# Performance work log

Measured on AMD Instinct MI355X. Metric: run time of the kernel, lower is better.

Reference implementation:

```python
import jax, jax.numpy as jnp
import numpy as np

EMB = 512
HEAD = 64
B, S = 4, 4096


def setup_inputs() -> dict:
    key = jax.random.key(0)
    kq, kk, kv, kwq, kwk, kwv = jax.random.split(key, 6)
    q = jax.random.normal(kq, (B, S, EMB), dtype=jnp.float32)
    k = jax.random.normal(kk, (B, S, EMB), dtype=jnp.float32)
    v = jax.random.normal(kv, (B, S, EMB), dtype=jnp.float32)
    # nn.Linear weights: [out_features, in_features], no bias
    sc = 1.0 / np.sqrt(EMB)
    Wq = jax.random.uniform(kwq, (HEAD, EMB), jnp.float32, -sc, sc)
    Wk = jax.random.uniform(kwk, (HEAD, EMB), jnp.float32, -sc, sc)
    Wv = jax.random.uniform(kwv, (HEAD, EMB), jnp.float32, -sc, sc)
    return {"q": q, "k": k, "v": v, "Wq": Wq, "Wk": Wk, "Wv": Wv}


def reference(q, k, v, Wq, Wk, Wv):
    scale = 1.0 / np.sqrt(HEAD).astype(np.float32)
    Q = jnp.einsum('bse,he->bsh', q, Wq)  # [B,S,HEAD]
    K = jnp.einsum('bse,he->bsh', k, Wk)
    V = jnp.einsum('bse,he->bsh', v, Wv)
    scores = jnp.einsum('bqh,bkh->bqk', Q, K) * scale  # [B,S,S]
    attn = jax.nn.softmax(scores, axis=-1)
    # dropout p=0.0 -> identity
    out = jnp.einsum('bqk,bkh->bqh', attn, V)  # [B,S,HEAD]
    return out
```

## Files before the change

kernel.cpp:

```cpp
#include <hip/hip_runtime.h>
#include <hip/hip_bf16.h>

#define EMB    512
#define HEAD   64
#define SEQ    4096
#define NB     4
#define NSPLIT 8
#define LDX    72

#define SL2E   0.18033688011112042f

typedef __bf16 bf16x8 __attribute__((ext_vector_type(8)));
typedef float  f32x4  __attribute__((ext_vector_type(4)));

__device__ inline ushort4 cvt4(float4 v) {
    __hip_bfloat16 a = __float2bfloat16(v.x), b = __float2bfloat16(v.y);
    __hip_bfloat16 c = __float2bfloat16(v.z), d = __float2bfloat16(v.w);
    ushort4 r;
    r.x = *(unsigned short*)&a; r.y = *(unsigned short*)&b;
    r.z = *(unsigned short*)&c; r.w = *(unsigned short*)&d;
    return r;
}

__global__ __launch_bounds__(256) void cvtw_kernel(
    const float* __restrict__ Wq, const float* __restrict__ Wk,
    const float* __restrict__ Wv, __hip_bfloat16* __restrict__ Wc)
{
    int idx   = blockIdx.x * 256 + threadIdx.x;
    int which = idx >> 13;
    int off   = (idx & 8191) * 4;
    const float* src = (which == 0) ? Wq : (which == 1) ? Wk : Wv;
    float s = (which == 0) ? SL2E : 1.0f;
    float4 v = *(const float4*)(src + off);
    v.x *= s; v.y *= s; v.z *= s; v.w *= s;
    *(ushort4*)(Wc + which * 64 * EMB + off) = cvt4(v);
}

__global__ __launch_bounds__(256, 3) void proj_kernel(
    const float* __restrict__ q, const float* __restrict__ k, const float* __restrict__ v,
    const __hip_bfloat16* __restrict__ Wc,
    __hip_bfloat16* __restrict__ Qo, __hip_bfloat16* __restrict__ Ko,
    __hip_bfloat16* __restrict__ Vto)
{
    __shared__ __hip_bfloat16 Xs[64][LDX];

    const int which = blockIdx.y;
    const float* __restrict__ x = (which == 0) ? q : (which == 1) ? k : v;
    const __hip_bfloat16* __restrict__ W = Wc + which * 64 * EMB;

    const int tid  = threadIdx.x;
    const int wave = tid >> 6, lane = tid & 63;
    const int l16  = lane & 15, quad = lane >> 4;
    const int r0   = blockIdx.x * 64;
    const float* __restrict__ xb = x + (size_t)r0 * EMB;

    const int sr = tid >> 4;
    const int sc = (tid & 15) << 2;

    const f32x4 z = {0.f, 0.f, 0.f, 0.f};
    f32x4 acc[4] = {z, z, z, z};

    float4 xr[4];
    bf16x8 wf[8];

#define LOADX(dst, e0)                                                        \
    _Pragma("unroll")                                                         \
    for (int it = 0; it < 4; ++it)                                            \
        dst[it] = *(const float4*)(xb + (size_t)(it * 16 + sr) * EMB + (e0) + sc);

#define LOADW(dst, e0)                                                        \
    _Pragma("unroll")                                                         \
    for (int st = 0; st < 2; ++st)                                            \
        _Pragma("unroll")                                                     \
        for (int t = 0; t < 4; ++t)                                           \
            dst[st * 4 + t] = *(const bf16x8*)(W + (size_t)(t * 16 + l16) * EMB \
                                               + (e0) + st * 32 + quad * 8);

    LOADX(xr, 0);
    LOADW(wf, 0);

    #pragma unroll
    for (int c = 0; c < 8; ++c) {
        const int e0 = c * 64;
        if (c) __syncthreads();
        #pragma unroll
        for (int it = 0; it < 4; ++it)
            *(ushort4*)&Xs[it * 16 + sr][sc] = cvt4(xr[it]);
        __syncthreads();

        bf16x8 a0 = *(const bf16x8*)&Xs[wave * 16 + l16][quad * 8];
        bf16x8 a1 = *(const bf16x8*)&Xs[wave * 16 + l16][32 + quad * 8];

        float4 xr2[4];
        bf16x8 wf2[8];
        if (c < 7) { LOADX(xr2, e0 + 64); LOADW(wf2, e0 + 64); }

        #pragma unroll
        for (int t = 0; t < 4; ++t)
            acc[t] = __builtin_amdgcn_mfma_f32_16x16x32_bf16(a0, wf[t], acc[t], 0, 0, 0);
        #pragma unroll
        for (int t = 0; t < 4; ++t)
            acc[t] = __builtin_amdgcn_mfma_f32_16x16x32_bf16(a1, wf[4 + t], acc[t], 0, 0, 0);

        if (c < 7) {
            #pragma unroll
            for (int it = 0; it < 4; ++it) xr[it] = xr2[it];
            #pragma unroll
            for (int j = 0; j < 8; ++j) wf[j] = wf2[j];
        }
    }
#undef LOADX
#undef LOADW

    #pragma unroll
    for (int t = 0; t < 4; ++t) {
        #pragma unroll
        for (int r = 0; r < 4; ++r) {
            int row = r0 + wave * 16 + quad * 4 + r;
            int h   = t * 16 + l16;
            __hip_bfloat16 val = __float2bfloat16(acc[t][r]);
            if (which == 0) {
                Qo[(size_t)row * HEAD + h] = val;
            } else if (which == 1) {
                Ko[(size_t)row * HEAD + h] = val;
            } else {
                int b = row >> 12, s = row & (SEQ - 1);
                Vto[((size_t)b * HEAD + h) * SEQ + s] = val;
            }
        }
    }
}

__global__ __launch_bounds__(256) void attn_kernel(
    const __hip_bfloat16* __restrict__ Qb, const __hip_bfloat16* __restrict__ Kb,
    const __hip_bfloat16* __restrict__ Vt, float* __restrict__ Op,
    float* __restrict__ lp)
{
    __shared__ __hip_bfloat16 QPs[64][LDX];
    __shared__ __hip_bfloat16 Ks[64][LDX];
    __shared__ __hip_bfloat16 Vs[64][LDX];

    const int tid  = threadIdx.x;
    const int wave = tid >> 6, lane = tid & 63;
    const int l16  = lane & 15, quad = lane >> 4;
    const int b    = blockIdx.y;
    const int q0   = blockIdx.x * 64;
    const int split = blockIdx.z;
    const int j0base = split * (SEQ / NSPLIT);

    for (int i = tid; i < 512; i += 256) {
        int r = i >> 3, c8 = (i & 7) * 8;
        *(uint4*)&QPs[r][c8] =
            *(const uint4*)(Qb + ((size_t)b * SEQ + q0 + r) * HEAD + c8);
    }
    __syncthreads();

    bf16x8 qf0 = *(const bf16x8*)&QPs[wave * 16 + l16][quad * 8];
    bf16x8 qf1 = *(const bf16x8*)&QPs[wave * 16 + l16][32 + quad * 8];

    const f32x4 z = {0.f, 0.f, 0.f, 0.f};
    f32x4 oacc[4] = {z, z, z, z};
    float l_r[4] = {0.f, 0.f, 0.f, 0.f};

    for (int jt = 0; jt < SEQ / NSPLIT; jt += 64) {
        const int j0 = j0base + jt;
        __syncthreads();
        for (int i = tid; i < 512; i += 256) {
            int r = i >> 3, c8 = (i & 7) * 8;
            *(uint4*)&Ks[r][c8] =
                *(const uint4*)(Kb + ((size_t)b * SEQ + j0 + r) * HEAD + c8);
            *(uint4*)&Vs[r][c8] =
                *(const uint4*)(Vt + ((size_t)b * HEAD + r) * SEQ + j0 + c8);
        }
        __syncthreads();

        f32x4 sacc[4] = {z, z, z, z};
        #pragma unroll
        for (int st = 0; st < 2; ++st) {
            bf16x8 a = (st == 0) ? qf0 : qf1;
            #pragma unroll
            for (int t = 0; t < 4; ++t) {
                bf16x8 bK = *(const bf16x8*)&Ks[t * 16 + l16][st * 32 + quad * 8];
                sacc[t] = __builtin_amdgcn_mfma_f32_16x16x32_bf16(a, bK, sacc[t], 0, 0, 0);
            }
        }

        #pragma unroll
        for (int r = 0; r < 4; ++r) {
            float ls = 0.f;
            #pragma unroll
            for (int t = 0; t < 4; ++t) {
                float p = __builtin_amdgcn_exp2f(sacc[t][r]);
                ls += p;
                QPs[wave * 16 + quad * 4 + r][t * 16 + l16] = __float2bfloat16(p);
            }
            l_r[r] += ls;
        }

        #pragma unroll
        for (int st = 0; st < 2; ++st) {
            bf16x8 pf = *(const bf16x8*)&QPs[wave * 16 + l16][st * 32 + quad * 8];
            #pragma unroll
            for (int t = 0; t < 4; ++t) {
                bf16x8 vf = *(const bf16x8*)&Vs[t * 16 + l16][st * 32 + quad * 8];
                oacc[t] = __builtin_amdgcn_mfma_f32_16x16x32_bf16(pf, vf, oacc[t], 0, 0, 0);
            }
        }
    }

    #pragma unroll
    for (int r = 0; r < 4; ++r) {
        float s = l_r[r];
        #pragma unroll
        for (int off = 1; off < 16; off <<= 1) s += __shfl_xor(s, off);
        l_r[r] = s;
    }
    const size_t pb = (size_t)(split * NB + b) * SEQ;
    if (l16 == 0) {
        #pragma unroll
        for (int r = 0; r < 4; ++r)
            lp[pb + q0 + wave * 16 + quad * 4 + r] = l_r[r];
    }
    #pragma unroll
    for (int t = 0; t < 4; ++t)
        #pragma unroll
        for (int r = 0; r < 4; ++r)
            Op[(pb + q0 + wave * 16 + quad * 4 + r) * HEAD + t * 16 + l16] = oacc[t][r];
}

__global__ __launch_bounds__(256) void merge_kernel(
    const float* __restrict__ Op, const float* __restrict__ lp,
    float* __restrict__ out)
{
    int idx = blockIdx.x * 256 + threadIdx.x;
    int bq  = idx >> 4;
    int c4  = (idx & 15) * 4;
    float4 acc = {0.f, 0.f, 0.f, 0.f};
    float  l   = 0.f;
    #pragma unroll
    for (int s = 0; s < NSPLIT; ++s) {
        float4 o = *(const float4*)(Op + ((size_t)s * NB * SEQ + bq) * HEAD + c4);
        acc.x += o.x; acc.y += o.y; acc.z += o.z; acc.w += o.w;
        l += lp[(size_t)s * NB * SEQ + bq];
    }
    float inv = 1.f / l;
    float4 r = {acc.x * inv, acc.y * inv, acc.z * inv, acc.w * inv};
    *(float4*)(out + (size_t)bq * HEAD + c4) = r;
}

extern "C" void kernel_launch(void* const* d_in, const int* in_sizes, int n_in,
                              void* d_out, int out_size, void* d_ws, size_t ws_size,
                              hipStream_t stream) {
    const float* q  = (const float*)d_in[0];
    const float* k  = (const float*)d_in[1];
    const float* v  = (const float*)d_in[2];
    const float* Wq = (const float*)d_in[3];
    const float* Wk = (const float*)d_in[4];
    const float* Wv = (const float*)d_in[5];
    float* out = (float*)d_out;

    __hip_bfloat16* Qb = (__hip_bfloat16*)d_ws;
    __hip_bfloat16* Kb = Qb + (size_t)NB * SEQ * HEAD;
    __hip_bfloat16* Vt = Kb + (size_t)NB * SEQ * HEAD;
    __hip_bfloat16* Wc = Vt + (size_t)NB * SEQ * HEAD;
    float* Op = (float*)(Wc + 3 * 64 * EMB);
    float* lp = Op + (size_t)NSPLIT * NB * SEQ * HEAD;

    cvtw_kernel<<<96, 256, 0, stream>>>(Wq, Wk, Wv, Wc);

    dim3 pgrid(NB * SEQ / 64, 3);
    proj_kernel<<<pgrid, dim3(256), 0, stream>>>(q, k, v, Wc, Qb, Kb, Vt);

    dim3 agrid(SEQ / 64, NB, NSPLIT);
    attn_kernel<<<agrid, dim3(256), 0, stream>>>(Qb, Kb, Vt, Op, lp);

    merge_kernel<<<(NB * SEQ * 16) / 256, dim3(256), 0, stream>>>(Op, lp, out);
}
```

Measured before the change: 184.2 us.

## Load K/V fragments directly from global memory and compute row sums via MFMA

Drops the shared-memory staging of Q, K and V tiles and the two block-wide barriers per iteration; each wave now reads its MFMA operand fragments straight from global memory, relying on caches for reuse across the four waves. Row sums of P are now produced by an extra MFMA against a ones vector, taking the same bf16-rounded P as the PV product, instead of fp32 adds plus shuffle reductions. This removes barrier and LDS traffic but replaces coalesced tile loads with strided 16-byte per-lane global loads that each wave repeats, raising L1/L2 pressure and exposing load latency without explicit prefetch.

```diff
diff --git a/kernel.cpp b/kernel.cpp
--- a/kernel.cpp
+++ b/kernel.cpp
@@ -136,43 +136,33 @@
     const __hip_bfloat16* __restrict__ Vt, float* __restrict__ Op,
     float* __restrict__ lp)
 {
-    __shared__ __hip_bfloat16 QPs[64][LDX];
-    __shared__ __hip_bfloat16 Ks[64][LDX];
-    __shared__ __hip_bfloat16 Vs[64][LDX];
+    __shared__ __hip_bfloat16 Ps[64][LDX];
 
     const int tid  = threadIdx.x;
     const int wave = tid >> 6, lane = tid & 63;
     const int l16  = lane & 15, quad = lane >> 4;
     const int b    = blockIdx.y;
     const int q0   = blockIdx.x * 64;
-    const int split = blockIdx.z;
-    const int j0base = split * (SEQ / NSPLIT);
-
-    for (int i = tid; i < 512; i += 256) {
-        int r = i >> 3, c8 = (i & 7) * 8;
-        *(uint4*)&QPs[r][c8] =
-            *(const uint4*)(Qb + ((size_t)b * SEQ + q0 + r) * HEAD + c8);
-    }
-    __syncthreads();
-
-    bf16x8 qf0 = *(const bf16x8*)&QPs[wave * 16 + l16][quad * 8];
-    bf16x8 qf1 = *(const bf16x8*)&QPs[wave * 16 + l16][32 + quad * 8];
+    const int j0b  = blockIdx.z * (SEQ / NSPLIT);
+
+    const __hip_bfloat16* qrow = Qb + ((size_t)b * SEQ + q0 + wave * 16 + l16) * HEAD + quad * 8;
+    bf16x8 qf0 = *(const bf16x8*)(qrow);
+    bf16x8 qf1 = *(const bf16x8*)(qrow + 32);
+
+    const __hip_bfloat16* kbase = Kb + (size_t)b * SEQ * HEAD + quad * 8;
+    const __hip_bfloat16* vbase = Vt + ((size_t)b * HEAD + l16) * SEQ + quad * 8;
 
     const f32x4 z = {0.f, 0.f, 0.f, 0.f};
     f32x4 oacc[4] = {z, z, z, z};
-    float l_r[4] = {0.f, 0.f, 0.f, 0.f};
+    f32x4 lacc = z;
+
+    const __hip_bfloat16 one_bf = __float2bfloat16(1.0f);
+    bf16x8 ones;
+    #pragma unroll
+    for (int j = 0; j < 8; ++j) ones[j] = *(const __bf16*)&one_bf;
 
     for (int jt = 0; jt < SEQ / NSPLIT; jt += 64) {
-        const int j0 = j0base + jt;
-        __syncthreads();
-        for (int i = tid; i < 512; i += 256) {
-            int r = i >> 3, c8 = (i & 7) * 8;
-            *(uint4*)&Ks[r][c8] =
-                *(const uint4*)(Kb + ((size_t)b * SEQ + j0 + r) * HEAD + c8);
-            *(uint4*)&Vs[r][c8] =
-                *(const uint4*)(Vt + ((size_t)b * HEAD + r) * SEQ + j0 + c8);
-        }
-        __syncthreads();
+        const int j0 = j0b + jt;
 
         f32x4 sacc[4] = {z, z, z, z};
         #pragma unroll
@@ -180,46 +170,37 @@
             bf16x8 a = (st == 0) ? qf0 : qf1;
             #pragma unroll
             for (int t = 0; t < 4; ++t) {
-                bf16x8 bK = *(const bf16x8*)&Ks[t * 16 + l16][st * 32 + quad * 8];
-                sacc[t] = __builtin_amdgcn_mfma_f32_16x16x32_bf16(a, bK, sacc[t], 0, 0, 0);
+                bf16x8 kf = *(const bf16x8*)(kbase + (size_t)(j0 + t * 16 + l16) * HEAD + st * 32);
+                sacc[t] = __builtin_amdgcn_mfma_f32_16x16x32_bf16(a, kf, sacc[t], 0, 0, 0);
             }
         }
 
         #pragma unroll
         for (int r = 0; r < 4; ++r) {
-            float ls = 0.f;
             #pragma unroll
             for (int t = 0; t < 4; ++t) {
                 float p = __builtin_amdgcn_exp2f(sacc[t][r]);
-                ls += p;
-                QPs[wave * 16 + quad * 4 + r][t * 16 + l16] = __float2bfloat16(p);
-            }
-            l_r[r] += ls;
+                Ps[wave * 16 + quad * 4 + r][t * 16 + l16] = __float2bfloat16(p);
+            }
         }
 
         #pragma unroll
         for (int st = 0; st < 2; ++st) {
-            bf16x8 pf = *(const bf16x8*)&QPs[wave * 16 + l16][st * 32 + quad * 8];
+            bf16x8 pf = *(const bf16x8*)&Ps[wave * 16 + l16][st * 32 + quad * 8];
+            lacc = __builtin_amdgcn_mfma_f32_16x16x32_bf16(pf, ones, lacc, 0, 0, 0);
             #pragma unroll
             for (int t = 0; t < 4; ++t) {
-                bf16x8 vf = *(const bf16x8*)&Vs[t * 16 + l16][st * 32 + quad * 8];
+                bf16x8 vf = *(const bf16x8*)(vbase + (size_t)(t * 16) * SEQ + j0 + st * 32);
                 oacc[t] = __builtin_amdgcn_mfma_f32_16x16x32_bf16(pf, vf, oacc[t], 0, 0, 0);
             }
         }
     }
 
-    #pragma unroll
-    for (int r = 0; r < 4; ++r) {
-        float s = l_r[r];
-        #pragma unroll
-        for (int off = 1; off < 16; off <<= 1) s += __shfl_xor(s, off);
-        l_r[r] = s;
-    }
-    const size_t pb = (size_t)(split * NB + b) * SEQ;
+    const size_t pb = (size_t)(blockIdx.z * NB + b) * SEQ;
     if (l16 == 0) {
         #pragma unroll
         for (int r = 0; r < 4; ++r)
-            lp[pb + q0 + wave * 16 + quad * 4 + r] = l_r[r];
+            lp[pb + q0 + wave * 16 + quad * 4 + r] = lacc[r];
     }
     #pragma unroll
     for (int t = 0; t < 4; ++t)
```

Result: slower. 261.8 us (+42.2%).
